# Kernel tuning notes

Hardware: AMD Instinct MI355X
Metric: run time of the kernel (lower is better)

Reference implementation:

```python
import jax, jax.numpy as jnp
import numpy as np

N_NODES = 50000
N_EDGES = 800000
IN_C, HID_C, OUT_C, HEADS = 128, 32, 64, 8
NEG_SLOPE = 0.2


def gat_layer(x, src, dst, W, a_src, a_dst, bias, concat, num_nodes):
    # W: [F_in, H*C]; a_src, a_dst: [H, C]; bias: [H*C] or [C]
    H, C = a_src.shape
    h = (x @ W).reshape(num_nodes, H, C)                      # [N,H,C]
    e_src = (h * a_src).sum(-1)                               # [N,H]
    e_dst = (h * a_dst).sum(-1)                               # [N,H]
    e = jax.nn.leaky_relu(e_src[src] + e_dst[dst], NEG_SLOPE) # [E,H]
    # segment softmax over incoming edges of each destination node
    m = jax.ops.segment_max(e, dst, num_segments=num_nodes)   # [N,H]
    ex = jnp.exp(e - m[dst])
    den = jax.ops.segment_sum(ex, dst, num_segments=num_nodes)
    alpha = ex / (den[dst] + 1e-16)                           # [E,H]
    out = jax.ops.segment_sum(h[src] * alpha[..., None], dst, num_segments=num_nodes)  # [N,H,C]
    out = out.reshape(num_nodes, H * C) if concat else out.mean(axis=1)
    return out + bias


def setup_inputs() -> dict:
    key = jax.random.key(0)
    ks = jax.random.split(key, 10)
    x = jax.random.normal(ks[0], (N_NODES, IN_C), dtype=jnp.float32)
    edge_index = jax.random.randint(ks[1], (2, N_EDGES), 0, N_NODES, dtype=jnp.int64)
    s1 = (2.0 / (IN_C + HID_C * HEADS)) ** 0.5
    s2 = (2.0 / (HID_C * HEADS + OUT_C)) ** 0.5
    return {
        "x": x,
        "edge_index": edge_index,
        "W1": jax.random.normal(ks[2], (IN_C, HEADS * HID_C), dtype=jnp.float32) * s1,
        "a_src1": jax.random.normal(ks[3], (HEADS, HID_C), dtype=jnp.float32) * 0.1,
        "a_dst1": jax.random.normal(ks[4], (HEADS, HID_C), dtype=jnp.float32) * 0.1,
        "b1": jnp.zeros((HEADS * HID_C,), dtype=jnp.float32),
        "W2": jax.random.normal(ks[5], (HEADS * HID_C, OUT_C), dtype=jnp.float32) * s2,
        "a_src2": jax.random.normal(ks[6], (1, OUT_C), dtype=jnp.float32) * 0.1,
        "a_dst2": jax.random.normal(ks[7], (1, OUT_C), dtype=jnp.float32) * 0.1,
        "b2": jnp.zeros((OUT_C,), dtype=jnp.float32),
    }


def reference(x, edge_index, W1, a_src1, a_dst1, b1, W2, a_src2, a_dst2, b2):
    # add self-loops (PyG GATConv default)
    loops = jnp.arange(N_NODES, dtype=edge_index.dtype)
    src = jnp.concatenate([edge_index[0], loops])
    dst = jnp.concatenate([edge_index[1], loops])
    # dropout layers are identity in eval mode
    h = gat_layer(x, src, dst, W1, a_src1, a_dst1, b1, True, N_NODES)
    h = jax.nn.elu(h)
    out = gat_layer(h, src, dst, W2, a_src2, a_dst2, b2, False, N_NODES)
    return out
```

## Files before the change

kernel.cpp:

```cpp
#include <hip/hip_runtime.h>
#include <math.h>

#define N_NODES 50000
#define N_EDGES 800000
#define IN_C    128
#define HID_C   32
#define OUT_C   64
#define HEADS   8
#define F1      256
#define PAD     64
#define G1_BLOCKS 3125
#define NB_BKT  782
#define BK_CAP  1280
#define A_BLOCKS 128
#define E_PER_A  6250

typedef __bf16 bf16x8 __attribute__((ext_vector_type(8)));
typedef float  f32x4  __attribute__((ext_vector_type(4)));
typedef float  f32x2  __attribute__((ext_vector_type(2)));
typedef unsigned short us8 __attribute__((ext_vector_type(8)));

__device__ __forceinline__ unsigned short f2b(float f) {
    unsigned u = __float_as_uint(f);
    u += 0x7FFF + ((u >> 16) & 1);
    return (unsigned short)(u >> 16);
}
__device__ __forceinline__ float blo(unsigned u) { return __uint_as_float(u << 16); }
__device__ __forceinline__ float bhi(unsigned u) { return __uint_as_float(u & 0xffff0000u); }
__device__ __forceinline__ f32x2 up2(unsigned u) {
    f32x2 r; r.x = blo(u); r.y = bhi(u); return r;
}

__global__ void convert_w(const float* __restrict__ W1, const float* __restrict__ W2,
                          const float* __restrict__ a_src2, const float* __restrict__ a_dst2,
                          unsigned short* __restrict__ W1t, unsigned short* __restrict__ W2t,
                          float* __restrict__ w2s, float* __restrict__ w2d,
                          int* __restrict__ bk_cnt) {
    int gid = blockIdx.x * 256 + threadIdx.x;
    if (gid < NB_BKT) bk_cnt[gid] = 0;
    if (gid < 256) {
        float s = 0.f, dd = 0.f;
        for (int c = 0; c < OUT_C; c++) {
            float w = W2[gid * OUT_C + c];
            s  += w * a_src2[c];
            dd += w * a_dst2[c];
        }
        w2s[gid] = s; w2d[gid] = dd;
    }
    if (gid < 256 * 128) {
        int n = gid >> 7, k = gid & 127;
        W1t[gid] = f2b(W1[k * F1 + n]);
    } else if (gid < 256 * 128 + 64 * 256) {
        int o = gid - 256 * 128;
        int n = o >> 8, k = o & 255;
        W2t[o] = f2b(W2[k * OUT_C + n]);
    }
}

__global__ __launch_bounds__(256) void g1A(const float* __restrict__ x,
                                           const unsigned short* __restrict__ W1t,
                                           const float* __restrict__ a_src,
                                           const float* __restrict__ a_dst,
                                           unsigned short* __restrict__ h1b,
                                           float* __restrict__ e_src,
                                           float* __restrict__ e_dst,
                                           const int* __restrict__ ei,
                                           int* __restrict__ bk_cnt,
                                           unsigned* __restrict__ ebuf) {
    if (blockIdx.x < A_BLOCKS) {
        __shared__ int cnt[NB_BKT];
        __shared__ int pos[NB_BKT];
        const int tid = threadIdx.x;
        const int e0 = blockIdx.x * E_PER_A, e1 = e0 + E_PER_A;
        for (int k = tid; k < NB_BKT; k += 256) cnt[k] = 0;
        __syncthreads();
        for (int e = e0 + tid; e < e1; e += 256)
            atomicAdd(&cnt[ei[N_EDGES + e] >> 6], 1);
        __syncthreads();
        for (int k = tid; k < NB_BKT; k += 256) {
            int c = cnt[k];
            pos[k] = (c > 0) ? atomicAdd(&bk_cnt[k], c) : 0;
        }
        __syncthreads();
        for (int e = e0 + tid; e < e1; e += 256) {
            int s = ei[e];
            int d = ei[N_EDGES + e];
            int k = d >> 6;
            int idx = atomicAdd(&pos[k], 1);
            ebuf[k * BK_CAP + idx] = ((unsigned)(d & 63) << 16) | (unsigned)s;
        }
        return;
    }
    const int t = threadIdx.x;
    const int wave = t >> 6, lane = t & 63;
    const int mlane = lane & 15, quad = lane >> 4;
    const int row0 = (blockIdx.x - A_BLOCKS) * 16;
    const int col0 = wave * 64;
    const float* xr = x + (size_t)(row0 + mlane) * IN_C;
    bf16x8 afr[4];
#pragma unroll
    for (int kc = 0; kc < 4; kc++) {
        float4 f0 = *(const float4*)&xr[kc * 32 + quad * 8];
        float4 f1 = *(const float4*)&xr[kc * 32 + quad * 8 + 4];
        us8 u;
        u[0] = f2b(f0.x); u[1] = f2b(f0.y); u[2] = f2b(f0.z); u[3] = f2b(f0.w);
        u[4] = f2b(f1.x); u[5] = f2b(f1.y); u[6] = f2b(f1.z); u[7] = f2b(f1.w);
        afr[kc] = __builtin_bit_cast(bf16x8, u);
    }
    f32x4 c[4];
#pragma unroll
    for (int nt = 0; nt < 4; nt++) c[nt] = (f32x4){0.f, 0.f, 0.f, 0.f};
#pragma unroll
    for (int kc = 0; kc < 4; kc++) {
#pragma unroll
        for (int nt = 0; nt < 4; nt++) {
            int col = col0 + nt * 16 + mlane;
            uint4 bw = *(const uint4*)&W1t[(size_t)col * IN_C + kc * 32 + quad * 8];
            bf16x8 b = __builtin_bit_cast(bf16x8, bw);
            c[nt] = __builtin_amdgcn_mfma_f32_16x16x32_bf16(afr[kc], b, c[nt], 0, 0, 0);
        }
    }
#pragma unroll
    for (int nt = 0; nt < 4; nt++) {
#pragma unroll
        for (int r = 0; r < 4; r++) {
            int gr = row0 + quad * 4 + r;
            h1b[(size_t)gr * F1 + col0 + nt * 16 + mlane] = f2b(c[nt][r]);
        }
    }
    float asA0 = a_src[col0 + mlane],      asA1 = a_src[col0 + 16 + mlane];
    float asB0 = a_src[col0 + 32 + mlane], asB1 = a_src[col0 + 48 + mlane];
    float adA0 = a_dst[col0 + mlane],      adA1 = a_dst[col0 + 16 + mlane];
    float adB0 = a_dst[col0 + 32 + mlane], adB1 = a_dst[col0 + 48 + mlane];
#pragma unroll
    for (int r = 0; r < 4; r++) {
        float psA = c[0][r] * asA0 + c[1][r] * asA1;
        float pdA = c[0][r] * adA0 + c[1][r] * adA1;
        float psB = c[2][r] * asB0 + c[3][r] * asB1;
        float pdB = c[2][r] * adB0 + c[3][r] * adB1;
#pragma unroll
        for (int off = 1; off < 16; off <<= 1) {
            psA += __shfl_xor(psA, off, 64);
            pdA += __shfl_xor(pdA, off, 64);
            psB += __shfl_xor(psB, off, 64);
            pdB += __shfl_xor(pdB, off, 64);
        }
        if (mlane == 0) {
            int gr = row0 + quad * 4 + r;
            e_src[gr * HEADS + wave * 2]     = psA;
            e_src[gr * HEADS + wave * 2 + 1] = psB;
            e_dst[gr * HEADS + wave * 2]     = pdA;
            e_dst[gr * HEADS + wave * 2 + 1] = pdB;
        }
    }
}

__global__ __launch_bounds__(256) void csrB(const unsigned* __restrict__ ebuf,
                                            const int* __restrict__ bk_cnt,
                                            int* __restrict__ deg,
                                            unsigned short* __restrict__ ssrc) {
    __shared__ int cnt[64];
    const int k = blockIdx.x;
    const int n0 = k << 6;
    const int tid = threadIdx.x;
    if (tid < 64) {
        int v = n0 + tid;
        if (v < N_NODES) {
            cnt[tid] = 1;
            ssrc[(size_t)v * PAD] = (unsigned short)v;
        }
    }
    __syncthreads();
    const int nb = bk_cnt[k];
    for (int t = tid; t < nb; t += 256) {
        unsigned w = ebuf[k * BK_CAP + t];
        int dl = w >> 16;
        int slot = atomicAdd(&cnt[dl], 1);
        ssrc[(size_t)(n0 + dl) * PAD + slot] = (unsigned short)(w & 0xffff);
    }
    __syncthreads();
    if (tid < 64) {
        int v = n0 + tid;
        if (v < N_NODES) deg[v] = cnt[tid];
    }
}

__global__ __launch_bounds__(256) void agg1s(const unsigned short* __restrict__ h1b,
                                             const float* __restrict__ e_src,
                                             const float* __restrict__ e_dst,
                                             const int* __restrict__ deg,
                                             const unsigned short* __restrict__ ssrc,
                                             const float* __restrict__ b1,
                                             const float* __restrict__ w2s,
                                             const float* __restrict__ w2d,
                                             unsigned short* __restrict__ hhb,
                                             float* __restrict__ e_src2,
                                             float* __restrict__ e_dst2) {
    int v = (blockIdx.x * 256 + threadIdx.x) >> 6;
    int lane = threadIdx.x & 63;
    int half = lane >> 5, l32 = lane & 31;
    int c0 = l32 * 8, h_acc = l32 >> 2;
    int c2 = c0 << 1;
    int h_exp = l32 & 7, j_exp = l32 >> 3;
    const char* h1c = (const char*)h1b;
    const char* esc = (const char*)e_src;
    int d = deg[v];
    int beg = v * PAD;
    int s_all = (int)ssrc[beg + lane];
    float edh = e_dst[v * HEADS + h_exp];
    f32x2 acc[4];
#pragma unroll
    for (int k = 0; k < 4; k++) acc[k] = (f32x2){0.f, 0.f};
    float den = 0.f;
    int dm1 = d - 1;
    for (int k16 = 0; k16 < d; k16 += 16) {
        int slotA = k16 + half + 2 * j_exp;
        int slotB = slotA + 8;
        int sA = __shfl(s_all, (slotA < dm1 ? slotA : dm1), 64);
        int sB = __shfl(s_all, (slotB < dm1 ? slotB : dm1), 64);
        float eA = *(const float*)(esc + ((sA << 5) + (h_exp << 2))) + edh;
        float eB = *(const float*)(esc + ((sB << 5) + (h_exp << 2))) + edh;
        eA = fmaxf(eA, 0.2f * eA);
        eB = fmaxf(eB, 0.2f * eB);
        float wA = (slotA < d) ? __expf(eA) : 0.f;
        float wB = (slotB < d) ? __expf(eB) : 0.f;
        int s_j[8];
#pragma unroll
        for (int j = 0; j < 8; j++) {
            int slot = k16 + half + 2 * j;
            s_j[j] = __shfl(s_all, (slot < dm1 ? slot : dm1), 64);
        }
        float w_j[8];
#pragma unroll
        for (int j = 0; j < 4; j++) {
            w_j[j]     = __shfl(wA, (j << 3) | h_acc, 32);
            w_j[j + 4] = __shfl(wB, (j << 3) | h_acc, 32);
        }
        uint4 r[8];
#pragma unroll
        for (int j = 0; j < 8; j++)
            r[j] = *(const uint4*)(h1c + (((unsigned)s_j[j] << 9) + c2));
#pragma unroll
        for (int j = 0; j < 8; j++) {
            den += w_j[j];
            acc[0] += w_j[j] * up2(r[j].x);
            acc[1] += w_j[j] * up2(r[j].y);
            acc[2] += w_j[j] * up2(r[j].z);
            acc[3] += w_j[j] * up2(r[j].w);
        }
    }
    den += __shfl_xor(den, 32, 64);
#pragma unroll
    for (int k = 0; k < 4; k++) {
        acc[k].x += __shfl_xor(acc[k].x, 32, 64);
        acc[k].y += __shfl_xor(acc[k].y, 32, 64);
    }
    if (half == 0) {
        float dinv = 1.f / (den + 1e-16f);
        us8 o;
        float ps = 0.f, pd = 0.f;
#pragma unroll
        for (int k = 0; k < 4; k++) {
            float v0 = acc[k].x * dinv + b1[c0 + 2 * k];
            float v1 = acc[k].y * dinv + b1[c0 + 2 * k + 1];
            v0 = (v0 > 0.f) ? v0 : (__expf(v0) - 1.f);
            v1 = (v1 > 0.f) ? v1 : (__expf(v1) - 1.f);
            o[2 * k]     = f2b(v0);
            o[2 * k + 1] = f2b(v1);
            ps += v0 * w2s[c0 + 2 * k] + v1 * w2s[c0 + 2 * k + 1];
            pd += v0 * w2d[c0 + 2 * k] + v1 * w2d[c0 + 2 * k + 1];
        }
        *(us8*)&hhb[(size_t)v * F1 + c0] = o;
#pragma unroll
        for (int off = 1; off < 32; off <<= 1) {
            ps += __shfl_xor(ps, off, 32);
            pd += __shfl_xor(pd, off, 32);
        }
        if (l32 == 0) { e_src2[v] = ps; e_dst2[v] = pd; }
    }
}

__global__ __launch_bounds__(256) void gemm2_mfma(const unsigned short* __restrict__ hhb,
                                                  const unsigned short* __restrict__ W2t,
                                                  unsigned short* __restrict__ h2b) {
    __shared__ unsigned short A[16 * 264];
    const int t = threadIdx.x;
    const int wave = t >> 6, lane = t & 63;
    const int mlane = lane & 15, quad = lane >> 4;
    const int row0 = blockIdx.x * 16;
#pragma unroll
    for (int i = 0; i < 2; i++) {
        int u = t + i * 256;
        int row = u >> 5, seg = u & 31;
        uint4 w = *(const uint4*)&hhb[(size_t)(row0 + row) * F1 + seg * 8];
        *(uint4*)&A[row * 264 + seg * 8] = w;
    }
    __syncthreads();
    f32x4 cc = (f32x4){0.f, 0.f, 0.f, 0.f};
    const int col = wave * 16 + mlane;
#pragma unroll
    for (int kc = 0; kc < 8; kc++) {
        uint4 aw = *(const uint4*)&A[mlane * 264 + kc * 32 + quad * 8];
        bf16x8 a = __builtin_bit_cast(bf16x8, aw);
        uint4 bw = *(const uint4*)&W2t[(size_t)col * F1 + kc * 32 + quad * 8];
        bf16x8 b = __builtin_bit_cast(bf16x8, bw);
        cc = __builtin_amdgcn_mfma_f32_16x16x32_bf16(a, b, cc, 0, 0, 0);
    }
#pragma unroll
    for (int r = 0; r < 4; r++) {
        int gr = row0 + quad * 4 + r;
        h2b[(size_t)gr * OUT_C + wave * 16 + mlane] = f2b(cc[r]);
    }
}

__global__ __launch_bounds__(256) void agg2s(const unsigned short* __restrict__ h2b,
                                             const float* __restrict__ e_src,
                                             const float* __restrict__ e_dst,
                                             const int* __restrict__ deg,
                                             const unsigned short* __restrict__ ssrc,
                                             const float* __restrict__ b2,
                                             float* __restrict__ out) {
    int v = (blockIdx.x * 256 + threadIdx.x) >> 6;
    int lane = threadIdx.x & 63;
    int d = deg[v], beg = v * PAD, dm1 = d - 1;
    float ed = e_dst[v];
    int g = lane >> 3, l8 = lane & 7;
    int c0 = l8 * 8;
    int c2 = c0 << 1;
    const char* h2c = (const char*)h2b;
    const char* esc = (const char*)e_src;
    int s_raw = (int)ssrc[beg + lane];
    int s_cl = s_raw > N_NODES - 1 ? N_NODES - 1 : s_raw;
    float e_own = *(const float*)(esc + (s_cl << 2)) + ed;
    e_own = fmaxf(e_own, 0.2f * e_own);
    float w_own = (lane < d) ? __expf(e_own) : 0.f;
    int sj[6]; float wj[6];
#pragma unroll
    for (int j = 0; j < 6; j++) {
        int slot = 8 * j + g;
        int tc = slot < dm1 ? slot : dm1;
        sj[j] = __shfl(s_cl, tc, 64);
        float w = __shfl(w_own, tc, 64);
        wj[j] = (slot < d) ? w : 0.f;
    }
    uint4 r[6];
#pragma unroll
    for (int j = 0; j < 6; j++)
        r[j] = *(const uint4*)(h2c + ((sj[j] << 7) + c2));
    f32x2 acc[4];
#pragma unroll
    for (int k = 0; k < 4; k++) acc[k] = (f32x2){0.f, 0.f};
    float den = 0.f;
#pragma unroll
    for (int j = 0; j < 6; j++) {
        den += wj[j];
        acc[0] += wj[j] * up2(r[j].x);
        acc[1] += wj[j] * up2(r[j].y);
        acc[2] += wj[j] * up2(r[j].z);
        acc[3] += wj[j] * up2(r[j].w);
    }
    den += __shfl_xor(den, 8, 64);
    den += __shfl_xor(den, 16, 64);
    den += __shfl_xor(den, 32, 64);
#pragma unroll
    for (int k = 0; k < 4; k++) {
        acc[k].x += __shfl_xor(acc[k].x, 8, 64);
        acc[k].y += __shfl_xor(acc[k].y, 8, 64);
        acc[k].x += __shfl_xor(acc[k].x, 16, 64);
        acc[k].y += __shfl_xor(acc[k].y, 16, 64);
        acc[k].x += __shfl_xor(acc[k].x, 32, 64);
        acc[k].y += __shfl_xor(acc[k].y, 32, 64);
    }
    if (g == 0) {
        float dinv = 1.f / (den + 1e-16f);
        float4 lo, hi;
        lo.x = acc[0].x * dinv + b2[c0 + 0]; lo.y = acc[0].y * dinv + b2[c0 + 1];
        lo.z = acc[1].x * dinv + b2[c0 + 2]; lo.w = acc[1].y * dinv + b2[c0 + 3];
        hi.x = acc[2].x * dinv + b2[c0 + 4]; hi.y = acc[2].y * dinv + b2[c0 + 5];
        hi.z = acc[3].x * dinv + b2[c0 + 6]; hi.w = acc[3].y * dinv + b2[c0 + 7];
        *(float4*)&out[(size_t)v * OUT_C + c0] = lo;
        *(float4*)&out[(size_t)v * OUT_C + c0 + 4] = hi;
    }
}

extern "C" void kernel_launch(void* const* d_in, const int* in_sizes, int n_in,
                              void* d_out, int out_size, void* d_ws, size_t ws_size,
                              hipStream_t stream) {
    const float* x      = (const float*)d_in[0];
    const int*   ei     = (const int*)d_in[1];
    const float* W1     = (const float*)d_in[2];
    const float* a_src1 = (const float*)d_in[3];
    const float* a_dst1 = (const float*)d_in[4];
    const float* b1     = (const float*)d_in[5];
    const float* W2     = (const float*)d_in[6];
    const float* a_src2 = (const float*)d_in[7];
    const float* a_dst2 = (const float*)d_in[8];
    const float* b2     = (const float*)d_in[9];
    float* out = (float*)d_out;

    char* ws = (char*)d_ws;
    size_t off = 0;
    auto alloc = [&](size_t bytes) { void* p = ws + off; off = (off + bytes + 255) & ~(size_t)255; return p; };
    unsigned short* h1b = (unsigned short*)alloc((size_t)N_NODES * F1 * 2);
    unsigned short* hhb = (unsigned short*)alloc((size_t)N_NODES * F1 * 2);
    unsigned short* h2b = (unsigned short*)alloc((size_t)N_NODES * OUT_C * 2);
    unsigned short* W1t = (unsigned short*)alloc((size_t)256 * 128 * 2);
    unsigned short* W2t = (unsigned short*)alloc((size_t)64 * 256 * 2);
    float* w2s    = (float*)alloc((size_t)256 * 4);
    float* w2d    = (float*)alloc((size_t)256 * 4);
    float* e_src1 = (float*)alloc((size_t)N_NODES * HEADS * 4);
    float* e_dst1 = (float*)alloc((size_t)N_NODES * HEADS * 4);
    float* e_src2 = (float*)alloc((size_t)N_NODES * 4);
    float* e_dst2 = (float*)alloc((size_t)N_NODES * 4);
    int*   deg    = (int*)alloc((size_t)N_NODES * 4);
    unsigned short* ssrc = (unsigned short*)alloc((size_t)N_NODES * PAD * 2);
    int*   bk_cnt = (int*)alloc((size_t)NB_BKT * 4);
    unsigned* ebuf = (unsigned*)alloc((size_t)NB_BKT * BK_CAP * 4);
    (void)ws_size; (void)n_in; (void)in_sizes; (void)out_size;

    const int node_waves = (N_NODES + 3) / 4;

    convert_w<<<200, 256, 0, stream>>>(W1, W2, a_src2, a_dst2, W1t, W2t, w2s, w2d, bk_cnt);
    g1A<<<A_BLOCKS + G1_BLOCKS, 256, 0, stream>>>(x, W1t, a_src1, a_dst1,
                                                  h1b, e_src1, e_dst1, ei, bk_cnt, ebuf);
    csrB<<<NB_BKT, 256, 0, stream>>>(ebuf, bk_cnt, deg, ssrc);
    agg1s<<<node_waves, 256, 0, stream>>>(h1b, e_src1, e_dst1, deg, ssrc, b1,
                                          w2s, w2d, hhb, e_src2, e_dst2);
    gemm2_mfma<<<G1_BLOCKS, 256, 0, stream>>>(hhb, W2t, h2b);
    agg2s<<<node_waves, 256, 0, stream>>>(h2b, e_src2, e_dst2, deg, ssrc, b2, out);
}
```

Before: 246.2 us.

## Regroup preprocessing kernels to merge edge bucketing with weight conversion and CSR with GEMM1

Edge bucketing now shares a launch with weight conversion and transposition, and the CSR build shares a launch with the first-layer GEMM, using block-index ranges to split the work. The bucket counter is zeroed with a memset instead of inside the conversion kernel. This goes from three launches to a memset plus two and lets independent work run concurrently. In exchange it adds a memset call, and the mixed kernels may be less balanced across blocks.

```diff
diff --git a/kernel.cpp b/kernel.cpp
--- a/kernel.cpp
+++ b/kernel.cpp
@@ -13,6 +13,7 @@
 #define NB_BKT  782
 #define BK_CAP  1280
 #define A_BLOCKS 128
+#define CW_BLOCKS 200
 #define E_PER_A  6250
 
 typedef __bf16 bf16x8 __attribute__((ext_vector_type(8)));
@@ -31,42 +32,12 @@
     f32x2 r; r.x = blo(u); r.y = bhi(u); return r;
 }
 
-__global__ void convert_w(const float* __restrict__ W1, const float* __restrict__ W2,
-                          const float* __restrict__ a_src2, const float* __restrict__ a_dst2,
-                          unsigned short* __restrict__ W1t, unsigned short* __restrict__ W2t,
-                          float* __restrict__ w2s, float* __restrict__ w2d,
-                          int* __restrict__ bk_cnt) {
-    int gid = blockIdx.x * 256 + threadIdx.x;
-    if (gid < NB_BKT) bk_cnt[gid] = 0;
-    if (gid < 256) {
-        float s = 0.f, dd = 0.f;
-        for (int c = 0; c < OUT_C; c++) {
-            float w = W2[gid * OUT_C + c];
-            s  += w * a_src2[c];
-            dd += w * a_dst2[c];
-        }
-        w2s[gid] = s; w2d[gid] = dd;
-    }
-    if (gid < 256 * 128) {
-        int n = gid >> 7, k = gid & 127;
-        W1t[gid] = f2b(W1[k * F1 + n]);
-    } else if (gid < 256 * 128 + 64 * 256) {
-        int o = gid - 256 * 128;
-        int n = o >> 8, k = o & 255;
-        W2t[o] = f2b(W2[k * OUT_C + n]);
-    }
-}
-
-__global__ __launch_bounds__(256) void g1A(const float* __restrict__ x,
-                                           const unsigned short* __restrict__ W1t,
-                                           const float* __restrict__ a_src,
-                                           const float* __restrict__ a_dst,
-                                           unsigned short* __restrict__ h1b,
-                                           float* __restrict__ e_src,
-                                           float* __restrict__ e_dst,
+__global__ __launch_bounds__(256) void cwA(const float* __restrict__ W1, const float* __restrict__ W2,
+                                           const float* __restrict__ a_src2, const float* __restrict__ a_dst2,
+                                           unsigned short* __restrict__ W1t, unsigned short* __restrict__ W2t,
+                                           float* __restrict__ w2s, float* __restrict__ w2d,
                                            const int* __restrict__ ei,
-                                           int* __restrict__ bk_cnt,
-                                           unsigned* __restrict__ ebuf) {
+                                           int* __restrict__ bk_cnt, unsigned* __restrict__ ebuf) {
     if (blockIdx.x < A_BLOCKS) {
         __shared__ int cnt[NB_BKT];
         __shared__ int pos[NB_BKT];
@@ -91,10 +62,68 @@
         }
         return;
     }
+    int gid = (blockIdx.x - A_BLOCKS) * 256 + threadIdx.x;
+    if (gid < 256) {
+        float s = 0.f, dd = 0.f;
+        for (int c = 0; c < OUT_C; c++) {
+            float w = W2[gid * OUT_C + c];
+            s  += w * a_src2[c];
+            dd += w * a_dst2[c];
+        }
+        w2s[gid] = s; w2d[gid] = dd;
+    }
+    if (gid < 256 * 128) {
+        int n = gid >> 7, k = gid & 127;
+        W1t[gid] = f2b(W1[k * F1 + n]);
+    } else if (gid < 256 * 128 + 64 * 256) {
+        int o = gid - 256 * 128;
+        int n = o >> 8, k = o & 255;
+        W2t[o] = f2b(W2[k * OUT_C + n]);
+    }
+}
+
+__global__ __launch_bounds__(256) void g1B(const float* __restrict__ x,
+                                           const unsigned short* __restrict__ W1t,
+                                           const float* __restrict__ a_src,
+                                           const float* __restrict__ a_dst,
+                                           unsigned short* __restrict__ h1b,
+                                           float* __restrict__ e_src,
+                                           float* __restrict__ e_dst,
+                                           const unsigned* __restrict__ ebuf,
+                                           const int* __restrict__ bk_cnt,
+                                           int* __restrict__ deg,
+                                           unsigned short* __restrict__ ssrc) {
+    if (blockIdx.x >= G1_BLOCKS) {
+        __shared__ int cnt[64];
+        const int k = blockIdx.x - G1_BLOCKS;
+        const int n0 = k << 6;
+        const int tid = threadIdx.x;
+        if (tid < 64) {
+            int v = n0 + tid;
+            if (v < N_NODES) {
+                cnt[tid] = 1;
+                ssrc[(size_t)v * PAD] = (unsigned short)v;
+            }
+        }
+        __syncthreads();
+        const int nb = bk_cnt[k];
+        for (int t = tid; t < nb; t += 256) {
+            unsigned w = ebuf[k * BK_CAP + t];
+            int dl = w >> 16;
+            int slot = atomicAdd(&cnt[dl], 1);
+            ssrc[(size_t)(n0 + dl) * PAD + slot] = (unsigned short)(w & 0xffff);
+        }
+        __syncthreads();
+        if (tid < 64) {
+            int v = n0 + tid;
+            if (v < N_NODES) deg[v] = cnt[tid];
+        }
+        return;
+    }
     const int t = threadIdx.x;
     const int wave = t >> 6, lane = t & 63;
     const int mlane = lane & 15, quad = lane >> 4;
-    const int row0 = (blockIdx.x - A_BLOCKS) * 16;
+    const int row0 = blockIdx.x * 16;
     const int col0 = wave * 64;
     const float* xr = x + (size_t)(row0 + mlane) * IN_C;
     bf16x8 afr[4];
@@ -152,36 +181,6 @@
             e_dst[gr * HEADS + wave * 2]     = pdA;
             e_dst[gr * HEADS + wave * 2 + 1] = pdB;
         }
-    }
-}
-
-__global__ __launch_bounds__(256) void csrB(const unsigned* __restrict__ ebuf,
-                                            const int* __restrict__ bk_cnt,
-                                            int* __restrict__ deg,
-                                            unsigned short* __restrict__ ssrc) {
-    __shared__ int cnt[64];
-    const int k = blockIdx.x;
-    const int n0 = k << 6;
-    const int tid = threadIdx.x;
-    if (tid < 64) {
-        int v = n0 + tid;
-        if (v < N_NODES) {
-            cnt[tid] = 1;
-            ssrc[(size_t)v * PAD] = (unsigned short)v;
-        }
-    }
-    __syncthreads();
-    const int nb = bk_cnt[k];
-    for (int t = tid; t < nb; t += 256) {
-        unsigned w = ebuf[k * BK_CAP + t];
-        int dl = w >> 16;
-        int slot = atomicAdd(&cnt[dl], 1);
-        ssrc[(size_t)(n0 + dl) * PAD + slot] = (unsigned short)(w & 0xffff);
-    }
-    __syncthreads();
-    if (tid < 64) {
-        int v = n0 + tid;
-        if (v < N_NODES) deg[v] = cnt[tid];
     }
 }
 
@@ -420,10 +419,12 @@
 
     const int node_waves = (N_NODES + 3) / 4;
 
-    convert_w<<<200, 256, 0, stream>>>(W1, W2, a_src2, a_dst2, W1t, W2t, w2s, w2d, bk_cnt);
-    g1A<<<A_BLOCKS + G1_BLOCKS, 256, 0, stream>>>(x, W1t, a_src1, a_dst1,
-                                                  h1b, e_src1, e_dst1, ei, bk_cnt, ebuf);
-    csrB<<<NB_BKT, 256, 0, stream>>>(ebuf, bk_cnt, deg, ssrc);
+    hipMemsetAsync(bk_cnt, 0, (size_t)NB_BKT * 4, stream);
+    cwA<<<A_BLOCKS + CW_BLOCKS, 256, 0, stream>>>(W1, W2, a_src2, a_dst2, W1t, W2t,
+                                                  w2s, w2d, ei, bk_cnt, ebuf);
+    g1B<<<G1_BLOCKS + NB_BKT, 256, 0, stream>>>(x, W1t, a_src1, a_dst1,
+                                                h1b, e_src1, e_dst1,
+                                                ebuf, bk_cnt, deg, ssrc);
     agg1s<<<node_waves, 256, 0, stream>>>(h1b, e_src1, e_dst1, deg, ssrc, b1,
                                           w2s, w2d, hhb, e_src2, e_dst2);
     gemm2_mfma<<<G1_BLOCKS, 256, 0, stream>>>(hhb, W2t, h2b);
```

After: 257.7 us. 1.05x slower.
